# Kernel tuning notes

Measured on AMD Instinct MI355X. Metric: run time of the kernel, lower is better.

The kernel has to match this reference:

```python
import jax, jax.numpy as jnp
import numpy as np
import math

B, S_IN, S_OUT, D_IN, D_OUT, G = 8, 1024, 1024, 96, 96, 8
LN_EPS = 1e-5


def setup_inputs() -> dict:
    key = jax.random.key(0)
    k_x, k_m, k_p, k_l = jax.random.split(key, 4)
    x = jax.random.normal(k_x, (B, S_IN, D_IN), dtype=jnp.float32)
    M = jax.random.uniform(k_m, (D_OUT, D_IN), minval=-0.5, maxval=0.5, dtype=jnp.float32)
    P = jax.random.uniform(k_p, (D_OUT, D_OUT, G), minval=-0.1, maxval=0.1, dtype=jnp.float32)
    Linker = jax.random.uniform(k_l, (S_IN, S_OUT), minval=-0.1, maxval=0.1, dtype=jnp.float32)
    gamma = jnp.ones((D_OUT,), dtype=jnp.float32)
    beta = jnp.zeros((D_OUT,), dtype=jnp.float32)
    return {"x": x, "M": M, "P": P, "Linker": Linker, "gamma": gamma, "beta": beta}


def _layer_norm(z, gamma, beta):
    mu = jnp.mean(z, axis=-1, keepdims=True)
    var = jnp.mean(jnp.square(z - mu), axis=-1, keepdims=True)
    return (z - mu) * jax.lax.rsqrt(var + LN_EPS) * gamma + beta


def reference(x, M, P, Linker, gamma, beta):
    # Z = x @ M^T, then LayerNorm over feature dim
    Z0 = jnp.einsum('bsj,ij->bsi', x, M)           # (B, S_in, D_out)
    Z = _layer_norm(Z0, gamma, beta)
    # periods[i,j,g] = i*(D_out*G) + j*G + g + 2
    periods = (jnp.arange(D_OUT * D_OUT * G, dtype=jnp.float32)
               .reshape(D_OUT, D_OUT, G) + 2.0)
    k = jnp.arange(S_IN, dtype=jnp.float32)
    # phi[s,i,j,g] = cos(2*pi*s / periods[i,j,g])
    phi = jnp.cos((2.0 * math.pi) * k[:, None, None, None] / periods[None])
    # fuse basis reduction: W[s,i,j] = sum_g P[i,j,g] * phi[s,i,j,g]
    W = jnp.einsum('sijg,ijg->sij', phi, P)        # (S_in, D_out, D_out)
    # T[b,s,i] = sum_j Z[b,s,j] * W[s,i,j]
    T = jnp.einsum('bsj,sij->bsi', Z, W)           # (B, S_in, D_out)
    # sequence transform via Linker
    U = jnp.einsum('bsi,st->bti', T, Linker)       # (B, S_out, D_out)
    # shared residual: x @ M^T (pre-LN) through the same Linker
    residual = jnp.einsum('bsi,st->bti', Z0, Linker)
    return U + residual
```

## Files before the change

kernel.cpp:

```cpp
#include <hip/hip_runtime.h>
#include <cstdint>
#include <cstddef>

#define BSTRIDE 98304

typedef __attribute__((ext_vector_type(8))) short short8;
typedef __attribute__((ext_vector_type(4))) float f32x4;

__device__ __forceinline__ uint16_t f2bf(float x) {
    uint32_t u = __float_as_uint(x);
    return (uint16_t)((u + 0x7FFF + ((u >> 16) & 1)) >> 16);
}
__device__ __forceinline__ float bf2f(uint16_t b) {
    return __uint_as_float(((uint32_t)b) << 16);
}

struct SmemS {
    union { float xs[8][96]; float zr[96][8]; } u;
    float zs[96][8];
    float part[4][8][96];
    uint16_t W[96][100];
    float ps1[8][12], ps2[8][12], stats[8][2];
};
union SmemF { SmemS f; struct { float T[64][65]; } kl; };

__global__ __launch_bounds__(384, 5) void k_fused(
    const float* __restrict__ x, const float* __restrict__ M,
    const float* __restrict__ P, const float* __restrict__ L,
    const float* __restrict__ gamma, const float* __restrict__ beta,
    uint16_t* __restrict__ Lt, uint16_t* __restrict__ Vt)
{
    __shared__ SmemF sm;
    const int t  = threadIdx.x;
    const int bx = blockIdx.x;

    if (bx >= 1024) {
        const int bx2 = bx - 1024;
        const int s0 = (bx2 & 15) * 64, t0 = (bx2 >> 4) * 64;
        if (t < 64) {
            for (int r = 0; r < 64; ++r)
                sm.kl.T[r][t] = L[(size_t)(s0 + r) * 1024 + t0 + t];
        }
        __syncthreads();
        if (t < 64) {
            uint16_t* orow = Lt + (size_t)(t0 + t) * 1024 + s0;
            #pragma unroll
            for (int c4 = 0; c4 < 16; ++c4) {
                uint32_t u01 = (uint32_t)f2bf(sm.kl.T[c4*4+0][t]) |
                               ((uint32_t)f2bf(sm.kl.T[c4*4+1][t]) << 16);
                uint32_t u23 = (uint32_t)f2bf(sm.kl.T[c4*4+2][t]) |
                               ((uint32_t)f2bf(sm.kl.T[c4*4+3][t]) << 16);
                uint2 o; o.x = u01; o.y = u23;
                *(uint2*)(orow + c4 * 4) = o;
            }
        }
        return;
    }

    const int s = bx;
    const int e = t % 96;
    const int q = t / 96;
    const int jq = q * 24;

    {
        float* xf = &sm.f.u.xs[0][0];
        #pragma unroll
        for (int r = 0; r < 2; ++r) {
            int idx = t + r * 384;
            int b = idx / 96, j = idx - b * 96;
            xf[idx] = x[(size_t)b * BSTRIDE + (size_t)s * 96 + j];
        }
    }
    __syncthreads();

    {
        float acc[8] = {0.f,0.f,0.f,0.f,0.f,0.f,0.f,0.f};
        const float* Mp = M + (size_t)e * 96 + jq;
        #pragma unroll
        for (int jj4 = 0; jj4 < 6; ++jj4) {
            float4 m4 = *(const float4*)(Mp + jj4 * 4);
            #pragma unroll
            for (int b = 0; b < 8; ++b) {
                float4 xv = *(const float4*)&sm.f.u.xs[b][jq + jj4 * 4];
                acc[b] = fmaf(m4.x, xv.x,
                         fmaf(m4.y, xv.y,
                         fmaf(m4.z, xv.z,
                         fmaf(m4.w, xv.w, acc[b]))));
            }
        }
        #pragma unroll
        for (int b = 0; b < 8; ++b) sm.f.part[q][b][e] = acc[b];
    }
    __syncthreads();

    {
        #pragma unroll
        for (int bb = 0; bb < 2; ++bb) {
            int b = q * 2 + bb;
            float v = sm.f.part[0][b][e] + sm.f.part[1][b][e] +
                      sm.f.part[2][b][e] + sm.f.part[3][b][e];
            sm.f.u.zr[e][b] = v;
        }
    }
    __syncthreads();

    if (t < 96) {
        const int b = t / 12, grp = t % 12;
        float s1 = 0.f, s2 = 0.f;
        #pragma unroll
        for (int k = 0; k < 8; ++k) {
            float v = sm.f.u.zr[grp * 8 + k][b];
            s1 += v; s2 += v * v;
        }
        sm.f.ps1[b][grp] = s1; sm.f.ps2[b][grp] = s2;
    }
    __syncthreads();
    if (t < 8) {
        float s1 = 0.f, s2 = 0.f;
        #pragma unroll
        for (int k = 0; k < 12; ++k) { s1 += sm.f.ps1[t][k]; s2 += sm.f.ps2[t][k]; }
        float mu  = s1 * (1.f / 96.f);
        float var = s2 * (1.f / 96.f) - mu * mu;
        sm.f.stats[t][0] = mu;
        sm.f.stats[t][1] = rsqrtf(var + 1e-5f);
    }
    __syncthreads();

    {
        float gm = gamma[e], bt = beta[e];
        #pragma unroll
        for (int bb = 0; bb < 2; ++bb) {
            int b = q * 2 + bb;
            sm.f.zs[e][b] =
                (sm.f.u.zr[e][b] - sm.f.stats[b][0]) * sm.f.stats[b][1] * gm + bt;
        }
    }

    {
        const float sf = (float)s;
        const int j = e;
        #pragma unroll 1
        for (int ii = 0; ii < 24; ii += 2) {
            const int i0 = q * 24 + ii;
            const float* Pp = P + ((size_t)i0 * 96 + j) * 8;
            float4 pa = *(const float4*)(Pp);
            float4 pb = *(const float4*)(Pp + 4);
            float4 pc = *(const float4*)(Pp + 768);
            float4 pd = *(const float4*)(Pp + 772);
            float pv0[8] = {pa.x, pa.y, pa.z, pa.w, pb.x, pb.y, pb.z, pb.w};
            float pv1[8] = {pc.x, pc.y, pc.z, pc.w, pd.x, pd.y, pd.z, pd.w};
            float base0 = (float)((i0 * 96 + j) * 8 + 2);
            float base1 = base0 + 768.0f;
            float w0 = 0.f, w1 = 0.f;
            #pragma unroll
            for (int g = 0; g < 8; ++g) {
                float inv0 = __builtin_amdgcn_rcpf(base0 + (float)g);
                float inv1 = __builtin_amdgcn_rcpf(base1 + (float)g);
                float a0 = sf * inv0; a0 -= floorf(a0);
                float a1 = sf * inv1; a1 -= floorf(a1);
                w0 = fmaf(pv0[g], __builtin_amdgcn_cosf(a0), w0);
                w1 = fmaf(pv1[g], __builtin_amdgcn_cosf(a1), w1);
            }
            *(uint32_t*)&sm.f.W[j][i0] =
                (uint32_t)f2bf(w0) | ((uint32_t)f2bf(w1) << 16);
        }
    }
    __syncthreads();

    {
        float tacc[8] = {0.f,0.f,0.f,0.f,0.f,0.f,0.f,0.f};
        #pragma unroll 4
        for (int jj = 0; jj < 24; ++jj) {
            int j = jq + jj;
            float w = bf2f(sm.f.W[j][e]);
            float4 z0 = *(const float4*)&sm.f.zs[j][0];
            float4 z1 = *(const float4*)&sm.f.zs[j][4];
            tacc[0] = fmaf(z0.x, w, tacc[0]);
            tacc[1] = fmaf(z0.y, w, tacc[1]);
            tacc[2] = fmaf(z0.z, w, tacc[2]);
            tacc[3] = fmaf(z0.w, w, tacc[3]);
            tacc[4] = fmaf(z1.x, w, tacc[4]);
            tacc[5] = fmaf(z1.y, w, tacc[5]);
            tacc[6] = fmaf(z1.z, w, tacc[6]);
            tacc[7] = fmaf(z1.w, w, tacc[7]);
        }
        #pragma unroll
        for (int b = 0; b < 8; ++b) sm.f.part[q][b][e] = tacc[b];
    }
    __syncthreads();

    {
        #pragma unroll
        for (int bb = 0; bb < 2; ++bb) {
            int b = q * 2 + bb;
            float T = sm.f.part[0][b][e] + sm.f.part[1][b][e] +
                      sm.f.part[2][b][e] + sm.f.part[3][b][e];
            float z0 = sm.f.u.zr[e][b];
            Vt[((size_t)b * 96 + e) * 1024 + s] = f2bf(T + z0);
        }
    }
}

__global__ __launch_bounds__(256) void k3_mfma(
    const uint16_t* __restrict__ Lt, const uint16_t* __restrict__ Vt,
    float* __restrict__ out)
{
    __shared__ float racc[3][64][25];
    const int lane = threadIdx.x & 63;
    const int kw   = threadIdx.x >> 6;
    const int m    = lane & 15;
    const int quad = lane >> 4;
    const int t0   = blockIdx.x * 16;
    const int b    = blockIdx.y;

    const uint16_t* Lp = Lt + (size_t)(t0 + m) * 1024 + kw * 256 + quad * 8;
    const uint16_t* Vp = Vt + ((size_t)b * 96 + m) * 1024 + kw * 256 + quad * 8;

    f32x4 acc[6];
    #pragma unroll
    for (int ii = 0; ii < 6; ++ii) acc[ii] = (f32x4){0.f, 0.f, 0.f, 0.f};

    short8 a = *(const short8*)Lp;
    short8 bv[6];
    #pragma unroll
    for (int ii = 0; ii < 6; ++ii)
        bv[ii] = *(const short8*)(Vp + (size_t)ii * 16 * 1024);

    for (int kc = 0; kc < 7; ++kc) {
        short8 an = *(const short8*)(Lp + (kc + 1) * 32);
        short8 bn[6];
        #pragma unroll
        for (int ii = 0; ii < 6; ++ii)
            bn[ii] = *(const short8*)(Vp + (size_t)ii * 16 * 1024 + (kc + 1) * 32);
        #pragma unroll
        for (int ii = 0; ii < 6; ++ii)
            acc[ii] = __builtin_amdgcn_mfma_f32_16x16x32_bf16(a, bv[ii], acc[ii], 0, 0, 0);
        a = an;
        #pragma unroll
        for (int ii = 0; ii < 6; ++ii) bv[ii] = bn[ii];
    }
    #pragma unroll
    for (int ii = 0; ii < 6; ++ii)
        acc[ii] = __builtin_amdgcn_mfma_f32_16x16x32_bf16(a, bv[ii], acc[ii], 0, 0, 0);

    if (kw > 0) {
        #pragma unroll
        for (int ii = 0; ii < 6; ++ii)
            #pragma unroll
            for (int r = 0; r < 4; ++r)
                racc[kw - 1][lane][ii * 4 + r] = acc[ii][r];
    }
    __syncthreads();
    if (kw == 0) {
        float* po = out + (size_t)b * BSTRIDE;
        #pragma unroll
        for (int ii = 0; ii < 6; ++ii)
            #pragma unroll
            for (int r = 0; r < 4; ++r)
                po[(size_t)(t0 + quad * 4 + r) * 96 + ii * 16 + m] =
                    acc[ii][r] + racc[0][lane][ii * 4 + r] +
                    racc[1][lane][ii * 4 + r] + racc[2][lane][ii * 4 + r];
    }
}

extern "C" void kernel_launch(void* const* d_in, const int* in_sizes, int n_in,
                              void* d_out, int out_size, void* d_ws, size_t ws_size,
                              hipStream_t stream)
{
    const float* x     = (const float*)d_in[0];
    const float* M     = (const float*)d_in[1];
    const float* P     = (const float*)d_in[2];
    const float* Lnk   = (const float*)d_in[3];
    const float* gamma = (const float*)d_in[4];
    const float* beta  = (const float*)d_in[5];
    float* out = (float*)d_out;

    uint8_t* ws = (uint8_t*)d_ws;
    uint16_t* Lt = (uint16_t*)ws;
    uint16_t* Vt = (uint16_t*)(ws + 2097152);

    k_fused <<<1280, 384, 0, stream>>>(x, M, P, Lnk, gamma, beta, Lt, Vt);
    k3_mfma <<<dim3(64, 8), 256, 0, stream>>>(Lt, Vt, out);
}
```

Measured before the change: 124.6 us.

## Split fused kernel and compute cosine basis via Chebyshev recurrence across positions

Measured after the change: 112.1 us. -10.1%, faster.

```diff
diff --git a/kernel.cpp b/kernel.cpp
--- a/kernel.cpp
+++ b/kernel.cpp
@@ -14,28 +14,34 @@
 __device__ __forceinline__ float bf2f(uint16_t b) {
     return __uint_as_float(((uint32_t)b) << 16);
 }
-
-struct SmemS {
-    union { float xs[8][96]; float zr[96][8]; } u;
-    float zs[96][8];
-    float part[4][8][96];
-    uint16_t W[96][100];
-    float ps1[8][12], ps2[8][12], stats[8][2];
+__device__ __forceinline__ float cosrev(float x) {
+    return __builtin_amdgcn_cosf(x);
+}
+
+union SmemA {
+    struct {
+        union {
+            float M[96][97];
+            struct { float zb[16][97]; float ps1[16][8];
+                     float ps2[16][8]; float stats[16][2]; } ln;
+        } m;
+        float xs[16][96];
+    } a;
+    struct { float T[64][65]; } kl;
 };
-union SmemF { SmemS f; struct { float T[64][65]; } kl; };
-
-__global__ __launch_bounds__(384, 5) void k_fused(
+
+__global__ __launch_bounds__(384, 4) void kA(
     const float* __restrict__ x, const float* __restrict__ M,
-    const float* __restrict__ P, const float* __restrict__ L,
+    const float* __restrict__ L,
     const float* __restrict__ gamma, const float* __restrict__ beta,
-    uint16_t* __restrict__ Lt, uint16_t* __restrict__ Vt)
+    float* __restrict__ Z0, float* __restrict__ Z, uint16_t* __restrict__ Lt)
 {
-    __shared__ SmemF sm;
+    __shared__ SmemA sm;
     const int t  = threadIdx.x;
     const int bx = blockIdx.x;
 
-    if (bx >= 1024) {
-        const int bx2 = bx - 1024;
+    if (bx >= 512) {
+        const int bx2 = bx - 512;
         const int s0 = (bx2 & 15) * 64, t0 = (bx2 >> 4) * 64;
         if (t < 64) {
             for (int r = 0; r < 64; ++r)
@@ -57,195 +63,235 @@
         return;
     }
 
-    const int s = bx;
+    const int R0 = bx * 16;
+    const int b  = R0 >> 10;
+    const int sb = R0 & 1023;
+
+    #pragma unroll
+    for (int k = 0; k < 6; ++k) {
+        int mm = t + 384 * k;
+        int i = mm / 24, j0 = (mm % 24) * 4;
+        float4 v = *(const float4*)(M + (size_t)i * 96 + j0);
+        sm.a.m.M[i][j0]   = v.x; sm.a.m.M[i][j0+1] = v.y;
+        sm.a.m.M[i][j0+2] = v.z; sm.a.m.M[i][j0+3] = v.w;
+    }
+    {
+        int row = t / 24, j0 = (t % 24) * 4;
+        float4 v = *(const float4*)(x + (size_t)(R0 + row) * 96 + j0);
+        *(float4*)&sm.a.xs[row][j0] = v;
+    }
+    __syncthreads();
+
     const int e = t % 96;
     const int q = t / 96;
-    const int jq = q * 24;
-
-    {
-        float* xf = &sm.f.u.xs[0][0];
-        #pragma unroll
-        for (int r = 0; r < 2; ++r) {
-            int idx = t + r * 384;
-            int b = idx / 96, j = idx - b * 96;
-            xf[idx] = x[(size_t)b * BSTRIDE + (size_t)s * 96 + j];
-        }
-    }
-    __syncthreads();
-
-    {
-        float acc[8] = {0.f,0.f,0.f,0.f,0.f,0.f,0.f,0.f};
-        const float* Mp = M + (size_t)e * 96 + jq;
-        #pragma unroll
-        for (int jj4 = 0; jj4 < 6; ++jj4) {
-            float4 m4 = *(const float4*)(Mp + jj4 * 4);
-            #pragma unroll
-            for (int b = 0; b < 8; ++b) {
-                float4 xv = *(const float4*)&sm.f.u.xs[b][jq + jj4 * 4];
-                acc[b] = fmaf(m4.x, xv.x,
-                         fmaf(m4.y, xv.y,
-                         fmaf(m4.z, xv.z,
-                         fmaf(m4.w, xv.w, acc[b]))));
-            }
-        }
-        #pragma unroll
-        for (int b = 0; b < 8; ++b) sm.f.part[q][b][e] = acc[b];
-    }
-    __syncthreads();
-
-    {
-        #pragma unroll
-        for (int bb = 0; bb < 2; ++bb) {
-            int b = q * 2 + bb;
-            float v = sm.f.part[0][b][e] + sm.f.part[1][b][e] +
-                      sm.f.part[2][b][e] + sm.f.part[3][b][e];
-            sm.f.u.zr[e][b] = v;
-        }
-    }
-    __syncthreads();
-
-    if (t < 96) {
-        const int b = t / 12, grp = t % 12;
+    float acc[4] = {0.f, 0.f, 0.f, 0.f};
+    for (int j0 = 0; j0 < 96; j0 += 4) {
+        float m0 = sm.a.m.M[e][j0+0], m1 = sm.a.m.M[e][j0+1];
+        float m2 = sm.a.m.M[e][j0+2], m3 = sm.a.m.M[e][j0+3];
+        #pragma unroll
+        for (int rr = 0; rr < 4; ++rr) {
+            float4 xv = *(const float4*)&sm.a.xs[q * 4 + rr][j0];
+            acc[rr] = fmaf(m0, xv.x, fmaf(m1, xv.y,
+                      fmaf(m2, xv.z, fmaf(m3, xv.w, acc[rr]))));
+        }
+    }
+    __syncthreads();
+    #pragma unroll
+    for (int rr = 0; rr < 4; ++rr) sm.a.m.ln.zb[q * 4 + rr][e] = acc[rr];
+    __syncthreads();
+
+    if (t < 128) {
+        int r = t >> 3, seg = t & 7;
         float s1 = 0.f, s2 = 0.f;
         #pragma unroll
-        for (int k = 0; k < 8; ++k) {
-            float v = sm.f.u.zr[grp * 8 + k][b];
+        for (int k = 0; k < 12; ++k) {
+            float v = sm.a.m.ln.zb[r][seg * 12 + k];
             s1 += v; s2 += v * v;
         }
-        sm.f.ps1[b][grp] = s1; sm.f.ps2[b][grp] = s2;
-    }
-    __syncthreads();
-    if (t < 8) {
+        sm.a.m.ln.ps1[r][seg] = s1; sm.a.m.ln.ps2[r][seg] = s2;
+    }
+    __syncthreads();
+    if (t < 16) {
         float s1 = 0.f, s2 = 0.f;
         #pragma unroll
-        for (int k = 0; k < 12; ++k) { s1 += sm.f.ps1[t][k]; s2 += sm.f.ps2[t][k]; }
+        for (int k = 0; k < 8; ++k) { s1 += sm.a.m.ln.ps1[t][k]; s2 += sm.a.m.ln.ps2[t][k]; }
         float mu  = s1 * (1.f / 96.f);
         float var = s2 * (1.f / 96.f) - mu * mu;
-        sm.f.stats[t][0] = mu;
-        sm.f.stats[t][1] = rsqrtf(var + 1e-5f);
+        sm.a.m.ln.stats[t][0] = mu;
+        sm.a.m.ln.stats[t][1] = rsqrtf(var + 1e-5f);
     }
     __syncthreads();
 
     {
         float gm = gamma[e], bt = beta[e];
         #pragma unroll
-        for (int bb = 0; bb < 2; ++bb) {
-            int b = q * 2 + bb;
-            sm.f.zs[e][b] =
-                (sm.f.u.zr[e][b] - sm.f.stats[b][0]) * sm.f.stats[b][1] * gm + bt;
-        }
+        for (int rr = 0; rr < 4; ++rr) {
+            int r = q * 4 + rr;
+            float z  = acc[rr];
+            float mu = sm.a.m.ln.stats[r][0], rs = sm.a.m.ln.stats[r][1];
+            size_t o = (size_t)(sb + r) * 768 + (size_t)b * 96 + e;
+            Z0[o] = z;
+            Z[o]  = (z - mu) * rs * gm + bt;
+        }
+    }
+}
+
+struct SmemB {
+    float    zs[8][8][100];
+    uint16_t W[8][12][104];
+    uint16_t stage[12][8][8];
+};
+
+__global__ __launch_bounds__(384, 4) void kB(
+    const float* __restrict__ P, const float* __restrict__ Z,
+    const float* __restrict__ Z0, uint16_t* __restrict__ Vt)
+{
+    __shared__ SmemB sm;
+    const int t  = threadIdx.x;
+    const int sg = blockIdx.x >> 3;
+    const int ih = blockIdx.x & 7;
+    const int s0 = sg * 8;
+    const int i0 = ih * 12;
+
+    #pragma unroll
+    for (int k = 0; k < 4; ++k) {
+        int c = t + 384 * k;
+        int elem = c * 4;
+        int sp = elem / 768, rem = elem - sp * 768;
+        int bb = rem / 96,  j0 = rem - bb * 96;
+        float4 v = *(const float4*)(Z + (size_t)s0 * 768 + elem);
+        *(float4*)&sm.zs[sp][bb][j0] = v;
     }
 
     {
-        const float sf = (float)s;
-        const int j = e;
+        const int j   = t % 96;
+        const int iqb = t / 96;
+        const float sf = (float)s0;
         #pragma unroll 1
-        for (int ii = 0; ii < 24; ii += 2) {
-            const int i0 = q * 24 + ii;
-            const float* Pp = P + ((size_t)i0 * 96 + j) * 8;
+        for (int kk = 0; kk < 3; ++kk) {
+            const int ip = kk * 4 + iqb;
+            const int ig = i0 + ip;
+            const float* Pp = P + ((size_t)ig * 96 + j) * 8;
             float4 pa = *(const float4*)(Pp);
             float4 pb = *(const float4*)(Pp + 4);
-            float4 pc = *(const float4*)(Pp + 768);
-            float4 pd = *(const float4*)(Pp + 772);
-            float pv0[8] = {pa.x, pa.y, pa.z, pa.w, pb.x, pb.y, pb.z, pb.w};
-            float pv1[8] = {pc.x, pc.y, pc.z, pc.w, pd.x, pd.y, pd.z, pd.w};
-            float base0 = (float)((i0 * 96 + j) * 8 + 2);
-            float base1 = base0 + 768.0f;
-            float w0 = 0.f, w1 = 0.f;
+            float pv[8] = {pa.x, pa.y, pa.z, pa.w, pb.x, pb.y, pb.z, pb.w};
+            float base = (float)((ig * 96 + j) * 8 + 2);
+            float c[8], cp[8], tc[8];
             #pragma unroll
             for (int g = 0; g < 8; ++g) {
-                float inv0 = __builtin_amdgcn_rcpf(base0 + (float)g);
-                float inv1 = __builtin_amdgcn_rcpf(base1 + (float)g);
-                float a0 = sf * inv0; a0 -= floorf(a0);
-                float a1 = sf * inv1; a1 -= floorf(a1);
-                w0 = fmaf(pv0[g], __builtin_amdgcn_cosf(a0), w0);
-                w1 = fmaf(pv1[g], __builtin_amdgcn_cosf(a1), w1);
+                float inv = __builtin_amdgcn_rcpf(base + (float)g);
+                tc[g] = 2.0f * cosrev(inv);
+                c[g]  = cosrev(__builtin_amdgcn_fractf(sf * inv));
+                cp[g] = cosrev(__builtin_amdgcn_fractf((sf - 1.0f) * inv));
             }
-            *(uint32_t*)&sm.f.W[j][i0] =
-                (uint32_t)f2bf(w0) | ((uint32_t)f2bf(w1) << 16);
+            #pragma unroll
+            for (int sp = 0; sp < 8; ++sp) {
+                float w = 0.f;
+                #pragma unroll
+                for (int g = 0; g < 8; ++g) w = fmaf(pv[g], c[g], w);
+                sm.W[sp][ip][j] = f2bf(w);
+                #pragma unroll
+                for (int g = 0; g < 8; ++g) {
+                    float cn = fmaf(tc[g], c[g], -cp[g]);
+                    cp[g] = c[g]; c[g] = cn;
+                }
+            }
         }
     }
     __syncthreads();
 
     {
-        float tacc[8] = {0.f,0.f,0.f,0.f,0.f,0.f,0.f,0.f};
-        #pragma unroll 4
-        for (int jj = 0; jj < 24; ++jj) {
-            int j = jq + jj;
-            float w = bf2f(sm.f.W[j][e]);
-            float4 z0 = *(const float4*)&sm.f.zs[j][0];
-            float4 z1 = *(const float4*)&sm.f.zs[j][4];
-            tacc[0] = fmaf(z0.x, w, tacc[0]);
-            tacc[1] = fmaf(z0.y, w, tacc[1]);
-            tacc[2] = fmaf(z0.z, w, tacc[2]);
-            tacc[3] = fmaf(z0.w, w, tacc[3]);
-            tacc[4] = fmaf(z1.x, w, tacc[4]);
-            tacc[5] = fmaf(z1.y, w, tacc[5]);
-            tacc[6] = fmaf(z1.z, w, tacc[6]);
-            tacc[7] = fmaf(z1.w, w, tacc[7]);
-        }
-        #pragma unroll
-        for (int b = 0; b < 8; ++b) sm.f.part[q][b][e] = tacc[b];
-    }
-    __syncthreads();
-
-    {
-        #pragma unroll
-        for (int bb = 0; bb < 2; ++bb) {
-            int b = q * 2 + bb;
-            float T = sm.f.part[0][b][e] + sm.f.part[1][b][e] +
-                      sm.f.part[2][b][e] + sm.f.part[3][b][e];
-            float z0 = sm.f.u.zr[e][b];
-            Vt[((size_t)b * 96 + e) * 1024 + s] = f2bf(T + z0);
-        }
-    }
-}
-
-__global__ __launch_bounds__(256) void k3_mfma(
+        const int s2  = t / 48;
+        const int rem = t % 48;
+        const int ipq = rem / 8;
+        const int bb  = rem % 8;
+        const int ia  = ipq * 2, ib = ia + 1;
+        float accA = 0.f, accB = 0.f;
+        const uint16_t* w0 = &sm.W[s2][ia][0];
+        const uint16_t* w1 = &sm.W[s2][ib][0];
+        const float*    zz = &sm.zs[s2][bb][0];
+        #pragma unroll 3
+        for (int j0 = 0; j0 < 96; j0 += 8) {
+            short8 wa = *(const short8*)(w0 + j0);
+            short8 wb = *(const short8*)(w1 + j0);
+            float4 z0 = *(const float4*)(zz + j0);
+            float4 z1 = *(const float4*)(zz + j0 + 4);
+            accA = fmaf(bf2f((uint16_t)wa[0]), z0.x, accA);
+            accB = fmaf(bf2f((uint16_t)wb[0]), z0.x, accB);
+            accA = fmaf(bf2f((uint16_t)wa[1]), z0.y, accA);
+            accB = fmaf(bf2f((uint16_t)wb[1]), z0.y, accB);
+            accA = fmaf(bf2f((uint16_t)wa[2]), z0.z, accA);
+            accB = fmaf(bf2f((uint16_t)wb[2]), z0.z, accB);
+            accA = fmaf(bf2f((uint16_t)wa[3]), z0.w, accA);
+            accB = fmaf(bf2f((uint16_t)wb[3]), z0.w, accB);
+            accA = fmaf(bf2f((uint16_t)wa[4]), z1.x, accA);
+            accB = fmaf(bf2f((uint16_t)wb[4]), z1.x, accB);
+            accA = fmaf(bf2f((uint16_t)wa[5]), z1.y, accA);
+            accB = fmaf(bf2f((uint16_t)wb[5]), z1.y, accB);
+            accA = fmaf(bf2f((uint16_t)wa[6]), z1.z, accA);
+            accB = fmaf(bf2f((uint16_t)wb[6]), z1.z, accB);
+            accA = fmaf(bf2f((uint16_t)wa[7]), z1.w, accA);
+            accB = fmaf(bf2f((uint16_t)wb[7]), z1.w, accB);
+        }
+        float2 r2 = *(const float2*)(Z0 + (size_t)(s0 + s2) * 768 + bb * 96 + i0 + ia);
+        sm.stage[ia][bb][s2] = f2bf(accA + r2.x);
+        sm.stage[ib][bb][s2] = f2bf(accB + r2.y);
+    }
+    __syncthreads();
+
+    if (t < 96) {
+        int ip = t >> 3, bb = t & 7;
+        uint4 v = *(const uint4*)&sm.stage[ip][bb][0];
+        *(uint4*)(Vt + ((size_t)bb * 96 + i0 + ip) * 1024 + s0) = v;
+    }
+}
+
+__global__ __launch_bounds__(256, 4) void k3_mfma(
     const uint16_t* __restrict__ Lt, const uint16_t* __restrict__ Vt,
     float* __restrict__ out)
 {
-    __shared__ float racc[3][64][25];
+    __shared__ float racc[3][64][13];
     const int lane = threadIdx.x & 63;
     const int kw   = threadIdx.x >> 6;
     const int m    = lane & 15;
     const int quad = lane >> 4;
     const int t0   = blockIdx.x * 16;
     const int b    = blockIdx.y;
+    const int ih   = blockIdx.z;
 
     const uint16_t* Lp = Lt + (size_t)(t0 + m) * 1024 + kw * 256 + quad * 8;
-    const uint16_t* Vp = Vt + ((size_t)b * 96 + m) * 1024 + kw * 256 + quad * 8;
-
-    f32x4 acc[6];
-    #pragma unroll
-    for (int ii = 0; ii < 6; ++ii) acc[ii] = (f32x4){0.f, 0.f, 0.f, 0.f};
+    const uint16_t* Vp = Vt + ((size_t)b * 96 + ih * 48 + m) * 1024 + kw * 256 + quad * 8;
+
+    f32x4 acc[3];
+    #pragma unroll
+    for (int ii = 0; ii < 3; ++ii) acc[ii] = (f32x4){0.f, 0.f, 0.f, 0.f};
 
     short8 a = *(const short8*)Lp;
-    short8 bv[6];
-    #pragma unroll
-    for (int ii = 0; ii < 6; ++ii)
+    short8 bv[3];
+    #pragma unroll
+    for (int ii = 0; ii < 3; ++ii)
         bv[ii] = *(const short8*)(Vp + (size_t)ii * 16 * 1024);
 
     for (int kc = 0; kc < 7; ++kc) {
         short8 an = *(const short8*)(Lp + (kc + 1) * 32);
-        short8 bn[6];
-        #pragma unroll
-        for (int ii = 0; ii < 6; ++ii)
+        short8 bn[3];
+        #pragma unroll
+        for (int ii = 0; ii < 3; ++ii)
             bn[ii] = *(const short8*)(Vp + (size_t)ii * 16 * 1024 + (kc + 1) * 32);
         #pragma unroll
-        for (int ii = 0; ii < 6; ++ii)
+        for (int ii = 0; ii < 3; ++ii)
             acc[ii] = __builtin_amdgcn_mfma_f32_16x16x32_bf16(a, bv[ii], acc[ii], 0, 0, 0);
         a = an;
         #pragma unroll
-        for (int ii = 0; ii < 6; ++ii) bv[ii] = bn[ii];
-    }
-    #pragma unroll
-    for (int ii = 0; ii < 6; ++ii)
+        for (int ii = 0; ii < 3; ++ii) bv[ii] = bn[ii];
+    }
+    #pragma unroll
+    for (int ii = 0; ii < 3; ++ii)
         acc[ii] = __builtin_amdgcn_mfma_f32_16x16x32_bf16(a, bv[ii], acc[ii], 0, 0, 0);
 
     if (kw > 0) {
         #pragma unroll
-        for (int ii = 0; ii < 6; ++ii)
+        for (int ii = 0; ii < 3; ++ii)
             #pragma unroll
             for (int r = 0; r < 4; ++r)
                 racc[kw - 1][lane][ii * 4 + r] = acc[ii][r];
@@ -254,10 +300,10 @@
     if (kw == 0) {
         float* po = out + (size_t)b * BSTRIDE;
         #pragma unroll
-        for (int ii = 0; ii < 6; ++ii)
+        for (int ii = 0; ii < 3; ++ii)
             #pragma unroll
             for (int r = 0; r < 4; ++r)
-                po[(size_t)(t0 + quad * 4 + r) * 96 + ii * 16 + m] =
+                po[(size_t)(t0 + quad * 4 + r) * 96 + ih * 48 + ii * 16 + m] =
                     acc[ii][r] + racc[0][lane][ii * 4 + r] +
                     racc[1][lane][ii * 4 + r] + racc[2][lane][ii * 4 + r];
     }
@@ -278,7 +324,10 @@
     uint8_t* ws = (uint8_t*)d_ws;
     uint16_t* Lt = (uint16_t*)ws;
     uint16_t* Vt = (uint16_t*)(ws + 2097152);
-
-    k_fused <<<1280, 384, 0, stream>>>(x, M, P, Lnk, gamma, beta, Lt, Vt);
-    k3_mfma <<<dim3(64, 8), 256, 0, stream>>>(Lt, Vt, out);
-}
+    float*    Z0 = (float*)(ws + 3670016);
+    float*    Z  = (float*)(ws + 6815744);
+
+    kA<<<768, 384, 0, stream>>>(x, M, Lnk, gamma, beta, Z0, Z, Lt);
+    kB<<<1024, 384, 0, stream>>>(P, Z, Z0, Vt);
+    k3_mfma<<<dim3(64, 8, 2), 256, 0, stream>>>(Lt, Vt, out);
+}
```
